# Performance work log

Hardware: AMD Instinct MI355X
Metric: run time of the kernel (lower is better)

Reference implementation:

```python
import jax, jax.numpy as jnp
import numpy as np


def setup_inputs() -> dict:
    key = jax.random.key(0)
    k1, k2 = jax.random.split(key)
    B, L, D = 8, 8192, 1024
    hidden_states = jax.random.normal(k1, (B, L, D), dtype=jnp.float32)
    boundary_mask = jax.random.randint(k2, (B, L), 0, 2).astype(bool)
    return {"hidden_states": hidden_states, "boundary_mask": boundary_mask}


def reference(hidden_states, boundary_mask):
    # Compact boundary-selected tokens to the front of each sequence.
    B, L, D = hidden_states.shape
    num_tokens = boundary_mask.sum(axis=-1)                     # [B]
    # next_max_seqlen is data-dependent; computed eagerly (host int), as in the
    # torch reference which calls int(num_tokens.max()).
    next_max_seqlen = int(jnp.max(num_tokens))
    # selected tokens keep their position; unselected get +L so a stable
    # argsort pushes them to the back while preserving order of selected ones
    token_idx = jnp.arange(L)[None, :] + (~boundary_mask).astype(jnp.int32) * L  # [B, L]
    seq_sorted_indices = jnp.argsort(token_idx, axis=1)          # [B, L]
    gather_idx = seq_sorted_indices[:, :next_max_seqlen, None]   # [B, M, 1]
    next_hidden_states = jnp.take_along_axis(
        hidden_states, jnp.broadcast_to(gather_idx, (B, next_max_seqlen, D)), axis=1
    )                                                            # [B, M, D]
    next_mask = jnp.arange(next_max_seqlen)[None, :] < num_tokens[:, None]  # [B, M]
    return (next_hidden_states, next_mask)
```

## Files before the change

kernel.cpp:

```cpp
#include <hip/hip_runtime.h>

#define BB 8
#define LL 8192
#define DD 1024

__global__ __launch_bounds__(1024) void build_perm(
    const int* __restrict__ mask, int* __restrict__ perm,
    float* __restrict__ mask_out, int S) {
  const int b = blockIdx.x;
  const int t = threadIdx.x;
  const int lane = t & 63;
  const int wave = t >> 6;

  __shared__ int wave_sums[16];
  __shared__ int s_total;

  const int* m = mask + (size_t)b * LL;
  const int base_i = t * 8;

  int vals[8];
  int local = 0;
#pragma unroll
  for (int k = 0; k < 8; ++k) {
    vals[k] = m[base_i + k] ? 1 : 0;
    local += vals[k];
  }

  int incl = local;
#pragma unroll
  for (int off = 1; off < 64; off <<= 1) {
    int up = __shfl_up(incl, off, 64);
    if (lane >= off) incl += up;
  }
  if (lane == 63) wave_sums[wave] = incl;
  __syncthreads();

  if (wave == 0 && lane < 16) {
    int v = wave_sums[lane];
#pragma unroll
    for (int off = 1; off < 16; off <<= 1) {
      int up = __shfl_up(v, off, 64);
      if (lane >= off) v += up;
    }
    wave_sums[lane] = v;
    if (lane == 15) s_total = v;
  }
  __syncthreads();

  const int wave_base = (wave == 0) ? 0 : wave_sums[wave - 1];
  const int num_tokens = s_total;
  int run = wave_base + incl - local;

#pragma unroll
  for (int k = 0; k < 8; ++k) {
    const int i = base_i + k;
    int dest;
    if (vals[k]) {
      dest = run;
      run += 1;
    } else {
      dest = num_tokens + (i - run);
    }
    if (dest < S) perm[(size_t)b * S + dest] = i;
  }

  for (int j = t; j < S; j += 1024) {
    mask_out[(size_t)b * S + j] = (j < num_tokens) ? 1.0f : 0.0f;
  }
}

__global__ __launch_bounds__(256) void gather_rows(
    const float* __restrict__ hidden, const int* __restrict__ perm,
    float* __restrict__ out, int S) {
  const int row = blockIdx.x;
  const int b = row / S;
  const int src = perm[row];
  const float4* __restrict__ in4 =
      (const float4*)(hidden + ((size_t)b * LL + (size_t)src) * DD);
  float4* __restrict__ out4 = (float4*)(out + (size_t)row * DD);
  out4[threadIdx.x] = in4[threadIdx.x];
}

extern "C" void kernel_launch(void* const* d_in, const int* in_sizes, int n_in,
                              void* d_out, int out_size, void* d_ws, size_t ws_size,
                              hipStream_t stream) {
  const float* hidden = (const float*)d_in[0];
  const int* mask = (const int*)d_in[1];

  const int S = out_size / (BB * (DD + 1));

  float* out_hidden = (float*)d_out;
  float* out_mask = out_hidden + (size_t)BB * S * DD;
  int* perm = (int*)d_ws;

  build_perm<<<BB, 1024, 0, stream>>>(mask, perm, out_mask, S);
  gather_rows<<<BB * S, 256, 0, stream>>>(hidden, perm, out_hidden, S);
}
```

Before: 369.6 us.

## Use persistent grid-stride gather with multiple rows per iteration and vectorized mask loads

Result: slower. 384.3 us (+4.0%).

```diff
diff --git a/kernel.cpp b/kernel.cpp
--- a/kernel.cpp
+++ b/kernel.cpp
@@ -3,6 +3,7 @@
 #define BB 8
 #define LL 8192
 #define DD 1024
+#define ROWS_PER_ITER 4
 
 __global__ __launch_bounds__(1024) void build_perm(
     const int* __restrict__ mask, int* __restrict__ perm,
@@ -18,13 +19,13 @@
   const int* m = mask + (size_t)b * LL;
   const int base_i = t * 8;
 
-  int vals[8];
+  int4 mv0 = ((const int4*)(m + base_i))[0];
+  int4 mv1 = ((const int4*)(m + base_i))[1];
+  int vals[8] = {mv0.x ? 1 : 0, mv0.y ? 1 : 0, mv0.z ? 1 : 0, mv0.w ? 1 : 0,
+                 mv1.x ? 1 : 0, mv1.y ? 1 : 0, mv1.z ? 1 : 0, mv1.w ? 1 : 0};
   int local = 0;
 #pragma unroll
-  for (int k = 0; k < 8; ++k) {
-    vals[k] = m[base_i + k] ? 1 : 0;
-    local += vals[k];
-  }
+  for (int k = 0; k < 8; ++k) local += vals[k];
 
   int incl = local;
 #pragma unroll
@@ -72,13 +73,33 @@
 __global__ __launch_bounds__(256) void gather_rows(
     const float* __restrict__ hidden, const int* __restrict__ perm,
     float* __restrict__ out, int S) {
-  const int row = blockIdx.x;
-  const int b = row / S;
-  const int src = perm[row];
-  const float4* __restrict__ in4 =
-      (const float4*)(hidden + ((size_t)b * LL + (size_t)src) * DD);
-  float4* __restrict__ out4 = (float4*)(out + (size_t)row * DD);
-  out4[threadIdx.x] = in4[threadIdx.x];
+  const int b = blockIdx.y;
+  const int t = threadIdx.x;
+  const float* __restrict__ src_base = hidden + (size_t)b * LL * DD;
+  float* __restrict__ dst_base = out + (size_t)b * S * DD;
+  const int* __restrict__ perm_b = perm + (size_t)b * S;
+  const int stride = gridDim.x * ROWS_PER_ITER;
+
+  for (int r0 = blockIdx.x * ROWS_PER_ITER; r0 < S; r0 += stride) {
+    int srcs[ROWS_PER_ITER];
+#pragma unroll
+    for (int u = 0; u < ROWS_PER_ITER; ++u) {
+      const int r = r0 + u;
+      srcs[u] = (r < S) ? perm_b[r] : -1;
+    }
+    float4 v[ROWS_PER_ITER];
+#pragma unroll
+    for (int u = 0; u < ROWS_PER_ITER; ++u) {
+      if (srcs[u] >= 0)
+        v[u] = ((const float4*)(src_base + (size_t)srcs[u] * DD))[t];
+    }
+#pragma unroll
+    for (int u = 0; u < ROWS_PER_ITER; ++u) {
+      const int r = r0 + u;
+      if (r < S)
+        ((float4*)(dst_base + (size_t)r * DD))[t] = v[u];
+    }
+  }
 }
 
 extern "C" void kernel_launch(void* const* d_in, const int* in_sizes, int n_in,
@@ -94,5 +115,5 @@
   int* perm = (int*)d_ws;
 
   build_perm<<<BB, 1024, 0, stream>>>(mask, perm, out_mask, S);
-  gather_rows<<<BB * S, 256, 0, stream>>>(hidden, perm, out_hidden, S);
+  gather_rows<<<dim3(256, BB), 256, 0, stream>>>(hidden, perm, out_hidden, S);
 }
```
